# Kernel tuning notes

Measured on AMD Instinct MI355X. Metric: run time of the kernel, lower is better.

The kernel has to match this reference:

```python
import jax, jax.numpy as jnp
import numpy as np

H = 512
V = 50000
S = 400
B = 64


def setup_inputs() -> dict:
    key = jax.random.key(0)
    ks = jax.random.split(key, 20)
    inp = {
        'input': jax.random.normal(ks[0], (1, B, H), jnp.float32),
        'encoder_states': jax.random.normal(ks[1], (S, B, H), jnp.float32),
        'oov_enc_mask': jax.random.randint(ks[2], (S, B), 0, 2, jnp.int32),
        'hidden': jnp.zeros((1, B, H), jnp.float32),
        # GRU params (PyTorch layout: gates ordered r, z, n)
        'W_ih': jax.random.normal(ks[3], (3 * H, H), jnp.float32) * 0.02,
        'W_hh': jax.random.normal(ks[4], (3 * H, H), jnp.float32) * 0.02,
        'b_ih': jax.random.normal(ks[5], (3 * H,), jnp.float32) * 0.02,
        'b_hh': jax.random.normal(ks[6], (3 * H,), jnp.float32) * 0.02,
        # output vocab projection Linear(2H, V)
        'out_W': jax.random.normal(ks[7], (V, 2 * H), jnp.float32) * 0.02,
        'out_b': jax.random.normal(ks[8], (V,), jnp.float32) * 0.02,
        # additive attention params
        'v': jax.random.normal(ks[9], (H, 1), jnp.float32) * 0.02,
        'Wh': jax.random.normal(ks[10], (H, H), jnp.float32) * 0.02,
        'Ws': jax.random.normal(ks[11], (H, H), jnp.float32) * 0.02,
        'b_attn': jax.random.normal(ks[12], (1, H), jnp.float32) * 0.02,
        # pointer probability Linears (H -> 1)
        'pWh': jax.random.normal(ks[13], (1, H), jnp.float32) * 0.02,
        'pWs': jax.random.normal(ks[14], (1, H), jnp.float32) * 0.02,
        'pWx': jax.random.normal(ks[15], (1, H), jnp.float32) * 0.02,
        'pWx_b': jax.random.normal(ks[16], (1,), jnp.float32) * 0.02,
    }
    return inp


def reference(input, encoder_states, oov_enc_mask, hidden,
              W_ih, W_hh, b_ih, b_hh, out_W, out_b,
              v, Wh, Ws, b_attn, pWh, pWs, pWx, pWx_b):
    x = input[0]            # (B, H)
    h0 = hidden[0]          # (B, H)

    # --- single-step GRU (PyTorch gate order r, z, n) ---
    gi = x @ W_ih.T + b_ih      # (B, 3H)
    gh = h0 @ W_hh.T + b_hh     # (B, 3H)
    ir, iz, inn = jnp.split(gi, 3, axis=1)
    hr, hz, hn = jnp.split(gh, 3, axis=1)
    r = jax.nn.sigmoid(ir + hr)
    z = jax.nn.sigmoid(iz + hz)
    n = jnp.tanh(inn + r * hn)
    h = (1.0 - z) * n + z * h0          # decoder_state, (B, H)
    hidden_new = h[None]                # (1, B, H)

    # --- Bahdanau additive attention, softmax over seq axis ---
    x1 = jnp.einsum('sbh,hk->sbk', encoder_states, Wh)   # (S, B, H)
    x2 = h @ Ws                                          # (B, H) broadcasts over S
    scores = jnp.squeeze(jnp.tanh(x1 + x2 + b_attn) @ v, 2)  # (S, B)
    attn = jax.nn.softmax(scores, axis=0)                # (S, B)
    attn_bs = attn.T                                     # (B, S)

    context = jnp.einsum('bs,sbh->bh', attn_bs, encoder_states)  # (B, H)
    global_state = jnp.concatenate([h, context], axis=1)         # (B, 2H)

    # --- pointer probability ---
    p = jax.nn.sigmoid(context @ pWh.T + h @ pWs.T + x @ pWx.T + pWx_b)  # (B, 1)

    vocab_distr = p * jax.nn.selu(global_state @ out_W.T + out_b)        # (B, V)
    oov_vocab_distr = (1.0 - p) * (attn_bs * oov_enc_mask.astype(jnp.float32).T)  # (B, S)
    extended_vocab_distr = jnp.concatenate([vocab_distr, oov_vocab_distr], axis=1)

    return extended_vocab_distr, hidden_new, jnp.squeeze(p), attn
```

## Files before the change

kernel.cpp:

```cpp
#include <hip/hip_runtime.h>
#include <cmath>

#define H    512
#define H2   1024
#define V    50000
#define SEQ  400
#define EXT  (V + SEQ)

typedef __attribute__((ext_vector_type(8))) short short8;
typedef __attribute__((ext_vector_type(4))) float floatx4;

#define LDS_BARRIER() asm volatile("s_waitcnt lgkmcnt(0)\n\ts_barrier" ::: "memory")

__device__ __forceinline__ unsigned int bfpack2(float lo, float hi) {
    unsigned int a = __float_as_uint(lo) + 0x8000u;
    unsigned int b = __float_as_uint(hi) + 0x8000u;
    return __builtin_amdgcn_perm(b, a, 0x07060302);
}
__device__ __forceinline__ uint4 pack8(float4 a, float4 b) {
    uint4 r;
    r.x = bfpack2(a.x, a.y);
    r.y = bfpack2(a.z, a.w);
    r.z = bfpack2(b.x, b.y);
    r.w = bfpack2(b.z, b.w);
    return r;
}
__device__ __forceinline__ float4 ld4(const float* p) { return *(const float4*)p; }

__global__ __launch_bounds__(256) void k0_transpose(
    const float* __restrict__ Wh, const float* __restrict__ Ws,
    unsigned short* __restrict__ WhT, unsigned short* __restrict__ WsT)
{
    __shared__ float T[64][65];
    const float* src = blockIdx.z ? Ws : Wh;
    unsigned short* dst = blockIdx.z ? WsT : WhT;
    const int k0 = blockIdx.x * 64, n0 = blockIdx.y * 64;
    const int tid = threadIdx.x;
    #pragma unroll
    for (int i = 0; i < 16; ++i) {
        int e = i * 256 + tid;
        int r = e >> 6, c = e & 63;
        T[r][c] = src[(size_t)(k0 + r) * H + n0 + c];
    }
    __syncthreads();
    #pragma unroll
    for (int i = 0; i < 16; ++i) {
        int e = i * 256 + tid;
        int nn = e >> 6, kk = e & 63;
        unsigned int u = __float_as_uint(T[kk][nn]) + 0x8000u;
        dst[(size_t)(n0 + nn) * H + k0 + kk] = (unsigned short)(u >> 16);
    }
}

__global__ __launch_bounds__(256) void k1_gru(
    const float* __restrict__ x, const float* __restrict__ h0,
    const float* __restrict__ W_ih, const float* __restrict__ W_hh,
    const float* __restrict__ b_ih, const float* __restrict__ b_hh,
    float* __restrict__ h_out)
{
    __shared__ uint4 Ax[512];
    __shared__ uint4 Ah[512];
    __shared__ uint4 Bg[6][512];
    const int tid  = threadIdx.x;
    const int wave = tid >> 6, lane = tid & 63;
    const int lrow = lane & 15, q = lane >> 4;
    const int J0   = blockIdx.x * 64;

    floatx4 acc[6][4];
    #pragma unroll
    for (int g = 0; g < 6; ++g)
        #pragma unroll
        for (int mt = 0; mt < 4; ++mt) acc[g][mt] = (floatx4){0.f, 0.f, 0.f, 0.f};

    for (int kc = 0; kc < H; kc += 64) {
        __syncthreads();
        #pragma unroll
        for (int c = 0; c < 2; ++c) {
            int idx = c * 256 + tid;
            int m = idx >> 3, j2 = idx & 7, k8 = j2 ^ (m & 7);
            const float* sx = x  + m * H + kc + k8 * 8;
            const float* sh = h0 + m * H + kc + k8 * 8;
            Ax[idx] = pack8(ld4(sx), ld4(sx + 4));
            Ah[idx] = pack8(ld4(sh), ld4(sh + 4));
        }
        #pragma unroll
        for (int g = 0; g < 6; ++g) {
            const float* Wb = (g < 3) ? W_ih : W_hh;
            const int go = (g % 3) * H;
            #pragma unroll
            for (int c = 0; c < 2; ++c) {
                int idx = c * 256 + tid;
                int n = idx >> 3, j2 = idx & 7, k8 = j2 ^ (n & 7);
                const float* sw = Wb + (size_t)(go + J0 + n) * H + kc + k8 * 8;
                Bg[g][idx] = pack8(ld4(sw), ld4(sw + 4));
            }
        }
        __syncthreads();
        #pragma unroll
        for (int kk8 = 0; kk8 < 8; kk8 += 4) {
            const int k8 = kk8 + q;
            short8 ax[4], ah[4];
            #pragma unroll
            for (int mt = 0; mt < 4; ++mt) {
                int m = mt * 16 + lrow;
                ax[mt] = *(const short8*)&Ax[m * 8 + (k8 ^ (m & 7))];
                ah[mt] = *(const short8*)&Ah[m * 8 + (k8 ^ (m & 7))];
            }
            const int n = wave * 16 + lrow;
            const int gidx = n * 8 + (k8 ^ (n & 7));
            #pragma unroll
            for (int g = 0; g < 6; ++g) {
                short8 bb = *(const short8*)&Bg[g][gidx];
                #pragma unroll
                for (int mt = 0; mt < 4; ++mt)
                    acc[g][mt] = __builtin_amdgcn_mfma_f32_16x16x32_bf16(
                        (g < 3) ? ax[mt] : ah[mt], bb, acc[g][mt], 0, 0, 0);
            }
        }
    }
    const int j = J0 + wave * 16 + lrow;
    const float bir = b_ih[j], biz = b_ih[H + j], bin = b_ih[2 * H + j];
    const float bhr = b_hh[j], bhz = b_hh[H + j], bhn = b_hh[2 * H + j];
    #pragma unroll
    for (int mt = 0; mt < 4; ++mt) {
        #pragma unroll
        for (int r = 0; r < 4; ++r) {
            const int bb = mt * 16 + q * 4 + r;
            float rg = 1.f / (1.f + expf(-(acc[0][mt][r] + bir + acc[3][mt][r] + bhr)));
            float zg = 1.f / (1.f + expf(-(acc[1][mt][r] + biz + acc[4][mt][r] + bhz)));
            float ng = tanhf(acc[2][mt][r] + bin + rg * (acc[5][mt][r] + bhn));
            float h0v = h0[bb * H + j];
            h_out[bb * H + j] = (1.f - zg) * ng + zg * h0v;
        }
    }
}

__global__ __launch_bounds__(256) void k2_x2(
    const float* __restrict__ h, const unsigned short* __restrict__ WsT,
    const float* __restrict__ b_attn, float* __restrict__ x2)
{
    __shared__ uint4 Ag[512];
    __shared__ uint4 Bgg[512];
    const int tid  = threadIdx.x;
    const int wave = tid >> 6, lane = tid & 63;
    const int lrow = lane & 15, q = lane >> 4;
    const int n0   = blockIdx.x * 64;

    floatx4 acc[4];
    #pragma unroll
    for (int mt = 0; mt < 4; ++mt) acc[mt] = (floatx4){0.f, 0.f, 0.f, 0.f};

    for (int kc = 0; kc < H; kc += 64) {
        __syncthreads();
        #pragma unroll
        for (int c = 0; c < 2; ++c) {
            int idx = c * 256 + tid;
            int m = idx >> 3, j2 = idx & 7, k8 = j2 ^ (m & 7);
            const float* sh = h + m * H + kc + k8 * 8;
            Ag[idx] = pack8(ld4(sh), ld4(sh + 4));
            int n = m, k8b = j2 ^ (n & 7);
            Bgg[idx] = *(const uint4*)(WsT + (size_t)(n0 + n) * H + kc + k8b * 8);
        }
        __syncthreads();
        #pragma unroll
        for (int kk8 = 0; kk8 < 8; kk8 += 4) {
            const int k8 = kk8 + q;
            const int n = wave * 16 + lrow;
            short8 bb = *(const short8*)&Bgg[n * 8 + (k8 ^ (n & 7))];
            #pragma unroll
            for (int mt = 0; mt < 4; ++mt) {
                int m = mt * 16 + lrow;
                short8 a = *(const short8*)&Ag[m * 8 + (k8 ^ (m & 7))];
                acc[mt] = __builtin_amdgcn_mfma_f32_16x16x32_bf16(a, bb, acc[mt], 0, 0, 0);
            }
        }
    }
    const int n = n0 + wave * 16 + lrow;
    const float ba = b_attn[n];
    #pragma unroll
    for (int mt = 0; mt < 4; ++mt)
        #pragma unroll
        for (int r = 0; r < 4; ++r) {
            const int bb = mt * 16 + q * 4 + r;
            x2[bb * H + n] = acc[mt][r] + ba;
        }
}

__global__ __launch_bounds__(256) void k3_scores(
    const float* __restrict__ enc, const unsigned short* __restrict__ WhT,
    const float* __restrict__ x2, const float* __restrict__ v,
    float* __restrict__ part)
{
    __shared__ uint4 AsG[2][512];
    __shared__ uint4 BsG[2][1024];
    __shared__ float red[256];
    const int s   = blockIdx.x;
    const int nc  = blockIdx.y;
    const int n0  = nc * 128;
    const int tid  = threadIdx.x;
    const int wave = tid >> 6, lane = tid & 63;
    const int lrow = lane & 15, q = lane >> 4;

    const float* Abase = enc + (size_t)s * 64 * H;

    float4 arA[2][2];
    uint4  arB[4];
    #pragma unroll
    for (int c = 0; c < 2; ++c) {
        int idx = c * 256 + tid;
        int m = idx >> 3, k8 = (idx & 7) ^ (m & 7);
        const float* sa = Abase + m * H + k8 * 8;
        arA[c][0] = ld4(sa); arA[c][1] = ld4(sa + 4);
    }
    #pragma unroll
    for (int c = 0; c < 4; ++c) {
        int idx = c * 256 + tid;
        int n = idx >> 3, k8 = (idx & 7) ^ (n & 7);
        arB[c] = *(const uint4*)(WhT + (size_t)(n0 + n) * H + k8 * 8);
    }

    floatx4 acc[4][2];
    #pragma unroll
    for (int mt = 0; mt < 4; ++mt)
        #pragma unroll
        for (int nt = 0; nt < 2; ++nt) acc[mt][nt] = (floatx4){0.f, 0.f, 0.f, 0.f};

    for (int kc = 0; kc < 8; ++kc) {
        const int buf = kc & 1;
        #pragma unroll
        for (int c = 0; c < 2; ++c)
            AsG[buf][c * 256 + tid] = pack8(arA[c][0], arA[c][1]);
        #pragma unroll
        for (int c = 0; c < 4; ++c)
            BsG[buf][c * 256 + tid] = arB[c];
        if (kc < 7) {
            const int ko = (kc + 1) * 64;
            #pragma unroll
            for (int c = 0; c < 2; ++c) {
                int idx = c * 256 + tid;
                int m = idx >> 3, k8 = (idx & 7) ^ (m & 7);
                const float* sa = Abase + m * H + ko + k8 * 8;
                arA[c][0] = ld4(sa); arA[c][1] = ld4(sa + 4);
            }
            #pragma unroll
            for (int c = 0; c < 4; ++c) {
                int idx = c * 256 + tid;
                int n = idx >> 3, k8 = (idx & 7) ^ (n & 7);
                arB[c] = *(const uint4*)(WhT + (size_t)(n0 + n) * H + ko + k8 * 8);
            }
        }
        LDS_BARRIER();
        #pragma unroll
        for (int kk8 = 0; kk8 < 8; kk8 += 4) {
            const int k8 = kk8 + q;
            short8 a[4], b[2];
            #pragma unroll
            for (int mt = 0; mt < 4; ++mt) {
                int m = mt * 16 + lrow;
                a[mt] = *(const short8*)&AsG[buf][m * 8 + (k8 ^ (m & 7))];
            }
            #pragma unroll
            for (int nt = 0; nt < 2; ++nt) {
                int n = wave * 32 + nt * 16 + lrow;
                b[nt] = *(const short8*)&BsG[buf][n * 8 + (k8 ^ (n & 7))];
            }
            #pragma unroll
            for (int mt = 0; mt < 4; ++mt)
                #pragma unroll
                for (int nt = 0; nt < 2; ++nt)
                    acc[mt][nt] = __builtin_amdgcn_mfma_f32_16x16x32_bf16(
                        a[mt], b[nt], acc[mt][nt], 0, 0, 0);
        }
    }
    float val[4][4];
    #pragma unroll
    for (int mt = 0; mt < 4; ++mt) {
        #pragma unroll
        for (int r = 0; r < 4; ++r) {
            const int bb = mt * 16 + q * 4 + r;
            float sum = 0.f;
            #pragma unroll
            for (int nt = 0; nt < 2; ++nt) {
                const int n = n0 + wave * 32 + nt * 16 + lrow;
                sum += tanhf(acc[mt][nt][r] + x2[bb * H + n]) * v[n];
            }
            #pragma unroll
            for (int off = 8; off > 0; off >>= 1) sum += __shfl_down(sum, off, 16);
            val[mt][r] = sum;
        }
    }
    __syncthreads();
    if (lrow == 0) {
        #pragma unroll
        for (int mt = 0; mt < 4; ++mt)
            #pragma unroll
            for (int r = 0; r < 4; ++r)
                red[wave * 64 + mt * 16 + q * 4 + r] = val[mt][r];
    }
    __syncthreads();
    if (tid < 64) {
        float sc = red[tid] + red[64 + tid] + red[128 + tid] + red[192 + tid];
        part[((size_t)nc * SEQ + s) * 64 + tid] = sc;
    }
}

__global__ __launch_bounds__(512) void k4_softmax(
    const float* __restrict__ part, float* __restrict__ attn_out)
{
    const int b = blockIdx.x;
    const int t = threadIdx.x;
    __shared__ float red[8];
    __shared__ float smax, ssum;
    float myv = 0.f, val = -1e30f;
    if (t < SEQ) {
        myv = part[((size_t)0 * SEQ + t) * 64 + b]
            + part[((size_t)1 * SEQ + t) * 64 + b]
            + part[((size_t)2 * SEQ + t) * 64 + b]
            + part[((size_t)3 * SEQ + t) * 64 + b];
        val = myv;
    }
    float m = val;
    #pragma unroll
    for (int off = 32; off > 0; off >>= 1) m = fmaxf(m, __shfl_down(m, off, 64));
    if ((t & 63) == 0) red[t >> 6] = m;
    __syncthreads();
    if (t == 0) {
        float mm = red[0];
        #pragma unroll
        for (int w = 1; w < 8; ++w) mm = fmaxf(mm, red[w]);
        smax = mm;
    }
    __syncthreads();
    float e = (t < SEQ) ? expf(myv - smax) : 0.f;
    float ssv = e;
    #pragma unroll
    for (int off = 32; off > 0; off >>= 1) ssv += __shfl_down(ssv, off, 64);
    if ((t & 63) == 0) red[t >> 6] = ssv;
    __syncthreads();
    if (t == 0) {
        float ss = 0.f;
        #pragma unroll
        for (int w = 0; w < 8; ++w) ss += red[w];
        ssum = ss;
    }
    __syncthreads();
    if (t < SEQ) attn_out[t * 64 + b] = e / ssum;
}

__global__ __launch_bounds__(128) void k5_context(
    const float* __restrict__ enc, const float* __restrict__ attn,
    float* __restrict__ ctxp)
{
    const int b  = blockIdx.x;
    const int hc = blockIdx.y;
    const int sg = blockIdx.z;
    const int t  = threadIdx.x;
    __shared__ float a_s[100];
    if (t < 100) a_s[t] = attn[(sg * 100 + t) * 64 + b];
    __syncthreads();
    const int hh = hc * 128 + t;
    const float* p = enc + ((size_t)(sg * 100) * 64 + b) * H + hh;
    float a0 = 0.f, a1 = 0.f;
    #pragma unroll 5
    for (int i = 0; i < 100; i += 2) {
        a0 += a_s[i]     * p[0];
        a1 += a_s[i + 1] * p[(size_t)64 * H];
        p += (size_t)128 * H;
    }
    ctxp[((size_t)sg * 64 + b) * H + hh] = a0 + a1;
}

__global__ __launch_bounds__(512) void k5b_p(
    const float* __restrict__ ctxp, const float* __restrict__ pWh,
    const float* __restrict__ hdec, const float* __restrict__ pWs,
    const float* __restrict__ x, const float* __restrict__ pWx,
    const float* __restrict__ pWx_b,
    float* __restrict__ ctx, float* __restrict__ p_out, float* __restrict__ p_ws)
{
    const int b = blockIdx.x;
    const int t = threadIdx.x;
    __shared__ float rbuf[8];
    float c = ctxp[((size_t)0 * 64 + b) * H + t]
            + ctxp[((size_t)1 * 64 + b) * H + t]
            + ctxp[((size_t)2 * 64 + b) * H + t]
            + ctxp[((size_t)3 * 64 + b) * H + t];
    ctx[b * H + t] = c;
    float term = c * pWh[t] + hdec[b * H + t] * pWs[t] + x[b * H + t] * pWx[t];
    #pragma unroll
    for (int off = 32; off > 0; off >>= 1) term += __shfl_down(term, off, 64);
    if ((t & 63) == 0) rbuf[t >> 6] = term;
    __syncthreads();
    if (t == 0) {
        float ssv = pWx_b[0];
        #pragma unroll
        for (int w = 0; w < 8; ++w) ssv += rbuf[w];
        float pv = 1.f / (1.f + expf(-ssv));
        p_out[b] = pv;
        p_ws[b]  = pv;
    }
}

__global__ __launch_bounds__(256) void k6_vocab(
    const float* __restrict__ h, const float* __restrict__ ctx,
    const float* __restrict__ outW, const float* __restrict__ outb,
    const float* __restrict__ p_ws, float* __restrict__ ext)
{
    __shared__ uint4 AsG[2][512];
    __shared__ uint4 BsG[2][512];
    __shared__ float p_l[64];
    const int tid  = threadIdx.x;
    const int wave = tid >> 6, lane = tid & 63;
    const int lrow = lane & 15, q = lane >> 4;
    const int v0   = blockIdx.x * 64;

    if (tid < 64) p_l[tid] = p_ws[tid];

    float4 arA[2][2], arB[2][2];
    {
        const float* Ab = h;
        #pragma unroll
        for (int c = 0; c < 2; ++c) {
            int idx = c * 256 + tid;
            int m = idx >> 3, k8 = (idx & 7) ^ (m & 7);
            const float* sa = Ab + m * H + k8 * 8;
            arA[c][0] = ld4(sa); arA[c][1] = ld4(sa + 4);
            int n = m, k8b = (idx & 7) ^ (n & 7);
            int vr = v0 + n; if (vr >= V) vr = V - 1;
            const float* sb = outW + (size_t)vr * H2 + k8b * 8;
            arB[c][0] = ld4(sb); arB[c][1] = ld4(sb + 4);
        }
    }

    floatx4 acc[4];
    #pragma unroll
    for (int mt = 0; mt < 4; ++mt) acc[mt] = (floatx4){0.f, 0.f, 0.f, 0.f};

    for (int kc = 0; kc < 16; ++kc) {
        const int buf = kc & 1;
        #pragma unroll
        for (int c = 0; c < 2; ++c) {
            AsG[buf][c * 256 + tid] = pack8(arA[c][0], arA[c][1]);
            BsG[buf][c * 256 + tid] = pack8(arB[c][0], arB[c][1]);
        }
        if (kc < 15) {
            const int ko = (kc + 1) * 64;
            const float* Ab = (ko < H) ? (h + ko) : (ctx + (ko - H));
            #pragma unroll
            for (int c = 0; c < 2; ++c) {
                int idx = c * 256 + tid;
                int m = idx >> 3, k8 = (idx & 7) ^ (m & 7);
                const float* sa = Ab + m * H + k8 * 8;
                arA[c][0] = ld4(sa); arA[c][1] = ld4(sa + 4);
                int n = m, k8b = (idx & 7) ^ (n & 7);
                int vr = v0 + n; if (vr >= V) vr = V - 1;
                const float* sb = outW + (size_t)vr * H2 + ko + k8b * 8;
                arB[c][0] = ld4(sb); arB[c][1] = ld4(sb + 4);
            }
        }
        LDS_BARRIER();
        #pragma unroll
        for (int kk8 = 0; kk8 < 8; kk8 += 4) {
            const int k8 = kk8 + q;
            const int n = wave * 16 + lrow;
            short8 b = *(const short8*)&BsG[buf][n * 8 + (k8 ^ (n & 7))];
            #pragma unroll
            for (int mt = 0; mt < 4; ++mt) {
                int m = mt * 16 + lrow;
                short8 a = *(const short8*)&AsG[buf][m * 8 + (k8 ^ (m & 7))];
                acc[mt] = __builtin_amdgcn_mfma_f32_16x16x32_bf16(a, b, acc[mt], 0, 0, 0);
            }
        }
    }
    const int n = v0 + wave * 16 + lrow;
    if (n < V) {
        const float ob = outb[n];
        #pragma unroll
        for (int mt = 0; mt < 4; ++mt) {
            #pragma unroll
            for (int r = 0; r < 4; ++r) {
                const int bb = mt * 16 + q * 4 + r;
                float zz = acc[mt][r] + ob;
                float sv = (zz > 0.f) ? 1.0507009873554805f * zz
                                      : 1.7580993408473766f * (expf(zz) - 1.f);
                ext[(size_t)bb * EXT + n] = p_l[bb] * sv;
            }
        }
    }
}

__global__ __launch_bounds__(256) void k7_oov(
    const float* __restrict__ attn, const int* __restrict__ mask,
    const float* __restrict__ p_ws, float* __restrict__ ext)
{
    int e = blockIdx.x * 256 + threadIdx.x;
    if (e < SEQ * 64) {
        int s = e >> 6, b = e & 63;
        float val = (1.f - p_ws[b]) * attn[e] * (mask[e] ? 1.f : 0.f);
        ext[(size_t)b * EXT + V + s] = val;
    }
}

extern "C" void kernel_launch(void* const* d_in, const int* in_sizes, int n_in,
                              void* d_out, int out_size, void* d_ws, size_t ws_size,
                              hipStream_t stream)
{
    (void)in_sizes; (void)n_in; (void)out_size; (void)ws_size;
    const float* x      = (const float*)d_in[0];
    const float* enc    = (const float*)d_in[1];
    const int*   mask   = (const int*)  d_in[2];
    const float* h0     = (const float*)d_in[3];
    const float* W_ih   = (const float*)d_in[4];
    const float* W_hh   = (const float*)d_in[5];
    const float* b_ih   = (const float*)d_in[6];
    const float* b_hh   = (const float*)d_in[7];
    const float* outW   = (const float*)d_in[8];
    const float* outb   = (const float*)d_in[9];
    const float* v      = (const float*)d_in[10];
    const float* Wh     = (const float*)d_in[11];
    const float* Ws     = (const float*)d_in[12];
    const float* b_attn = (const float*)d_in[13];
    const float* pWh    = (const float*)d_in[14];
    const float* pWs    = (const float*)d_in[15];
    const float* pWx    = (const float*)d_in[16];
    const float* pWx_b  = (const float*)d_in[17];

    float* out        = (float*)d_out;
    float* out_ext    = out;
    float* out_hidden = out + (size_t)64 * EXT;
    float* out_p      = out_hidden + 64 * H;
    float* out_attn   = out_p + 64;

    float* ws       = (float*)d_ws;
    float* ws_x2    = ws;
    float* ws_part  = ws_x2 + 64 * H;
    float* ws_ctxp  = ws_part + 4 * SEQ * 64;
    float* ws_ctx   = ws_ctxp + 4 * 64 * H;
    float* ws_p     = ws_ctx + 64 * H;
    unsigned short* ws_whT = (unsigned short*)(ws_p + 64);
    unsigned short* ws_wsT = ws_whT + (size_t)H * H;

    k0_transpose<<<dim3(8, 8, 2), 256, 0, stream>>>(Wh, Ws, ws_whT, ws_wsT);
    k1_gru<<<8, 256, 0, stream>>>(x, h0, W_ih, W_hh, b_ih, b_hh, out_hidden);
    k2_x2<<<8, 256, 0, stream>>>(out_hidden, ws_wsT, b_attn, ws_x2);
    k3_scores<<<dim3(SEQ, 4), 256, 0, stream>>>(enc, ws_whT, ws_x2, v, ws_part);
    k4_softmax<<<64, 512, 0, stream>>>(ws_part, out_attn);
    k5_context<<<dim3(64, 4, 4), 128, 0, stream>>>(enc, out_attn, ws_ctxp);
    k5b_p<<<64, 512, 0, stream>>>(ws_ctxp, pWh, out_hidden, pWs, x, pWx, pWx_b,
                                  ws_ctx, out_p, ws_p);
    k6_vocab<<<(V + 63) / 64, 256, 0, stream>>>(out_hidden, ws_ctx, outW, outb,
                                                ws_p, out_ext);
    k7_oov<<<(SEQ * 64 + 255) / 256, 256, 0, stream>>>(out_attn, mask, ws_p, out_ext);
}
```

Baseline: 520.0 us.

## Split GRU GEMM over K, drop register prefetch, widen vocab tiles

The GRU gate GEMM is split across 8 K-slices in a 2D grid. Partial sums go to a workspace buffer, and a new finalize kernel reduces them and applies the gate nonlinearities, so the 8-block GRU launch no longer underfills the GPU. The k3 scores and k6 vocab kernels lose their register-prefetch double buffering and return to simple single-buffered LDS loops. k6 now computes 128 vocab columns per block with two N-subtiles per wave, which reuses the activation tile more but overlaps loads with compute less and launches half as many blocks. The split GRU adds an extra kernel launch and roughly 6 MB of workspace traffic.

New measurement: 463.8 us. -10.8%, faster.

```diff
diff --git a/kernel.cpp b/kernel.cpp
--- a/kernel.cpp
+++ b/kernel.cpp
@@ -9,8 +9,6 @@
 
 typedef __attribute__((ext_vector_type(8))) short short8;
 typedef __attribute__((ext_vector_type(4))) float floatx4;
-
-#define LDS_BARRIER() asm volatile("s_waitcnt lgkmcnt(0)\n\ts_barrier" ::: "memory")
 
 __device__ __forceinline__ unsigned int bfpack2(float lo, float hi) {
     unsigned int a = __float_as_uint(lo) + 0x8000u;
@@ -52,11 +50,10 @@
     }
 }
 
-__global__ __launch_bounds__(256) void k1_gru(
+__global__ __launch_bounds__(256) void k1_gru_part(
     const float* __restrict__ x, const float* __restrict__ h0,
     const float* __restrict__ W_ih, const float* __restrict__ W_hh,
-    const float* __restrict__ b_ih, const float* __restrict__ b_hh,
-    float* __restrict__ h_out)
+    float* __restrict__ gacc)
 {
     __shared__ uint4 Ax[512];
     __shared__ uint4 Ah[512];
@@ -65,74 +62,96 @@
     const int wave = tid >> 6, lane = tid & 63;
     const int lrow = lane & 15, q = lane >> 4;
     const int J0   = blockIdx.x * 64;
-
-    floatx4 acc[6][4];
-    #pragma unroll
-    for (int g = 0; g < 6; ++g)
-        #pragma unroll
-        for (int mt = 0; mt < 4; ++mt) acc[g][mt] = (floatx4){0.f, 0.f, 0.f, 0.f};
-
-    for (int kc = 0; kc < H; kc += 64) {
-        __syncthreads();
+    const int ks   = blockIdx.y;
+    const int kc   = ks * 64;
+
+    #pragma unroll
+    for (int c = 0; c < 2; ++c) {
+        int idx = c * 256 + tid;
+        int m = idx >> 3, j2 = idx & 7, k8 = j2 ^ (m & 7);
+        const float* sx = x  + m * H + kc + k8 * 8;
+        const float* sh = h0 + m * H + kc + k8 * 8;
+        Ax[idx] = pack8(ld4(sx), ld4(sx + 4));
+        Ah[idx] = pack8(ld4(sh), ld4(sh + 4));
+    }
+    #pragma unroll
+    for (int g = 0; g < 6; ++g) {
+        const float* Wb = (g < 3) ? W_ih : W_hh;
+        const int go = (g % 3) * H;
         #pragma unroll
         for (int c = 0; c < 2; ++c) {
             int idx = c * 256 + tid;
-            int m = idx >> 3, j2 = idx & 7, k8 = j2 ^ (m & 7);
-            const float* sx = x  + m * H + kc + k8 * 8;
-            const float* sh = h0 + m * H + kc + k8 * 8;
-            Ax[idx] = pack8(ld4(sx), ld4(sx + 4));
-            Ah[idx] = pack8(ld4(sh), ld4(sh + 4));
-        }
+            int n = idx >> 3, j2 = idx & 7, k8 = j2 ^ (n & 7);
+            const float* sw = Wb + (size_t)(go + J0 + n) * H + kc + k8 * 8;
+            Bg[g][idx] = pack8(ld4(sw), ld4(sw + 4));
+        }
+    }
+    __syncthreads();
+
+    floatx4 acc[6];
+    #pragma unroll
+    for (int g = 0; g < 6; ++g) acc[g] = (floatx4){0.f, 0.f, 0.f, 0.f};
+    floatx4 accm[6][4];
+    #pragma unroll
+    for (int g = 0; g < 6; ++g)
+        #pragma unroll
+        for (int mt = 0; mt < 4; ++mt) accm[g][mt] = (floatx4){0.f, 0.f, 0.f, 0.f};
+
+    #pragma unroll
+    for (int kk8 = 0; kk8 < 8; kk8 += 4) {
+        const int k8 = kk8 + q;
+        short8 ax[4], ah[4];
+        #pragma unroll
+        for (int mt = 0; mt < 4; ++mt) {
+            int m = mt * 16 + lrow;
+            ax[mt] = *(const short8*)&Ax[m * 8 + (k8 ^ (m & 7))];
+            ah[mt] = *(const short8*)&Ah[m * 8 + (k8 ^ (m & 7))];
+        }
+        const int n = wave * 16 + lrow;
+        const int gidx = n * 8 + (k8 ^ (n & 7));
         #pragma unroll
         for (int g = 0; g < 6; ++g) {
-            const float* Wb = (g < 3) ? W_ih : W_hh;
-            const int go = (g % 3) * H;
-            #pragma unroll
-            for (int c = 0; c < 2; ++c) {
-                int idx = c * 256 + tid;
-                int n = idx >> 3, j2 = idx & 7, k8 = j2 ^ (n & 7);
-                const float* sw = Wb + (size_t)(go + J0 + n) * H + kc + k8 * 8;
-                Bg[g][idx] = pack8(ld4(sw), ld4(sw + 4));
-            }
-        }
-        __syncthreads();
-        #pragma unroll
-        for (int kk8 = 0; kk8 < 8; kk8 += 4) {
-            const int k8 = kk8 + q;
-            short8 ax[4], ah[4];
-            #pragma unroll
-            for (int mt = 0; mt < 4; ++mt) {
-                int m = mt * 16 + lrow;
-                ax[mt] = *(const short8*)&Ax[m * 8 + (k8 ^ (m & 7))];
-                ah[mt] = *(const short8*)&Ah[m * 8 + (k8 ^ (m & 7))];
-            }
-            const int n = wave * 16 + lrow;
-            const int gidx = n * 8 + (k8 ^ (n & 7));
-            #pragma unroll
-            for (int g = 0; g < 6; ++g) {
-                short8 bb = *(const short8*)&Bg[g][gidx];
-                #pragma unroll
-                for (int mt = 0; mt < 4; ++mt)
-                    acc[g][mt] = __builtin_amdgcn_mfma_f32_16x16x32_bf16(
-                        (g < 3) ? ax[mt] : ah[mt], bb, acc[g][mt], 0, 0, 0);
-            }
+            short8 bb = *(const short8*)&Bg[g][gidx];
+            #pragma unroll
+            for (int mt = 0; mt < 4; ++mt)
+                accm[g][mt] = __builtin_amdgcn_mfma_f32_16x16x32_bf16(
+                    (g < 3) ? ax[mt] : ah[mt], bb, accm[g][mt], 0, 0, 0);
         }
     }
     const int j = J0 + wave * 16 + lrow;
-    const float bir = b_ih[j], biz = b_ih[H + j], bin = b_ih[2 * H + j];
-    const float bhr = b_hh[j], bhz = b_hh[H + j], bhn = b_hh[2 * H + j];
-    #pragma unroll
-    for (int mt = 0; mt < 4; ++mt) {
-        #pragma unroll
-        for (int r = 0; r < 4; ++r) {
-            const int bb = mt * 16 + q * 4 + r;
-            float rg = 1.f / (1.f + expf(-(acc[0][mt][r] + bir + acc[3][mt][r] + bhr)));
-            float zg = 1.f / (1.f + expf(-(acc[1][mt][r] + biz + acc[4][mt][r] + bhz)));
-            float ng = tanhf(acc[2][mt][r] + bin + rg * (acc[5][mt][r] + bhn));
-            float h0v = h0[bb * H + j];
-            h_out[bb * H + j] = (1.f - zg) * ng + zg * h0v;
-        }
-    }
+    #pragma unroll
+    for (int g = 0; g < 6; ++g)
+        #pragma unroll
+        for (int mt = 0; mt < 4; ++mt)
+            #pragma unroll
+            for (int r = 0; r < 4; ++r) {
+                const int bb = mt * 16 + q * 4 + r;
+                gacc[(((size_t)g * 8 + ks) * 64 + bb) * H + j] = accm[g][mt][r];
+            }
+}
+
+__global__ __launch_bounds__(256) void k1_gru_fin(
+    const float* __restrict__ gacc, const float* __restrict__ h0,
+    const float* __restrict__ b_ih, const float* __restrict__ b_hh,
+    float* __restrict__ h_out)
+{
+    const int e = blockIdx.x * 256 + threadIdx.x;
+    const int j = e & (H - 1);
+    const int b = e >> 9;
+    float gs[6];
+    #pragma unroll
+    for (int g = 0; g < 6; ++g) {
+        float sum = 0.f;
+        #pragma unroll
+        for (int ks = 0; ks < 8; ++ks)
+            sum += gacc[(((size_t)g * 8 + ks) * 64 + b) * H + j];
+        gs[g] = sum;
+    }
+    float rg = 1.f / (1.f + expf(-(gs[0] + b_ih[j] + gs[3] + b_hh[j])));
+    float zg = 1.f / (1.f + expf(-(gs[1] + b_ih[H + j] + gs[4] + b_hh[H + j])));
+    float ng = tanhf(gs[2] + b_ih[2 * H + j] + rg * (gs[5] + b_hh[2 * H + j]));
+    float h0v = h0[b * H + j];
+    h_out[b * H + j] = (1.f - zg) * ng + zg * h0v;
 }
 
 __global__ __launch_bounds__(256) void k2_x2(
@@ -158,8 +177,7 @@
             int m = idx >> 3, j2 = idx & 7, k8 = j2 ^ (m & 7);
             const float* sh = h + m * H + kc + k8 * 8;
             Ag[idx] = pack8(ld4(sh), ld4(sh + 4));
-            int n = m, k8b = j2 ^ (n & 7);
-            Bgg[idx] = *(const uint4*)(WsT + (size_t)(n0 + n) * H + kc + k8b * 8);
+            Bgg[idx] = *(const uint4*)(WsT + (size_t)(n0 + m) * H + kc + k8 * 8);
         }
         __syncthreads();
         #pragma unroll
@@ -191,8 +209,8 @@
     const float* __restrict__ x2, const float* __restrict__ v,
     float* __restrict__ part)
 {
-    __shared__ uint4 AsG[2][512];
-    __shared__ uint4 BsG[2][1024];
+    __shared__ uint4 AsG[512];
+    __shared__ uint4 BsG[1024];
     __shared__ float red[256];
     const int s   = blockIdx.x;
     const int nc  = blockIdx.y;
@@ -201,55 +219,29 @@
     const int wave = tid >> 6, lane = tid & 63;
     const int lrow = lane & 15, q = lane >> 4;
 
+    floatx4 acc[4][2];
+    #pragma unroll
+    for (int mt = 0; mt < 4; ++mt)
+        #pragma unroll
+        for (int nt = 0; nt < 2; ++nt) acc[mt][nt] = (floatx4){0.f, 0.f, 0.f, 0.f};
+
     const float* Abase = enc + (size_t)s * 64 * H;
-
-    float4 arA[2][2];
-    uint4  arB[4];
-    #pragma unroll
-    for (int c = 0; c < 2; ++c) {
-        int idx = c * 256 + tid;
-        int m = idx >> 3, k8 = (idx & 7) ^ (m & 7);
-        const float* sa = Abase + m * H + k8 * 8;
-        arA[c][0] = ld4(sa); arA[c][1] = ld4(sa + 4);
-    }
-    #pragma unroll
-    for (int c = 0; c < 4; ++c) {
-        int idx = c * 256 + tid;
-        int n = idx >> 3, k8 = (idx & 7) ^ (n & 7);
-        arB[c] = *(const uint4*)(WhT + (size_t)(n0 + n) * H + k8 * 8);
-    }
-
-    floatx4 acc[4][2];
-    #pragma unroll
-    for (int mt = 0; mt < 4; ++mt)
-        #pragma unroll
-        for (int nt = 0; nt < 2; ++nt) acc[mt][nt] = (floatx4){0.f, 0.f, 0.f, 0.f};
-
-    for (int kc = 0; kc < 8; ++kc) {
-        const int buf = kc & 1;
-        #pragma unroll
-        for (int c = 0; c < 2; ++c)
-            AsG[buf][c * 256 + tid] = pack8(arA[c][0], arA[c][1]);
-        #pragma unroll
-        for (int c = 0; c < 4; ++c)
-            BsG[buf][c * 256 + tid] = arB[c];
-        if (kc < 7) {
-            const int ko = (kc + 1) * 64;
-            #pragma unroll
-            for (int c = 0; c < 2; ++c) {
-                int idx = c * 256 + tid;
-                int m = idx >> 3, k8 = (idx & 7) ^ (m & 7);
-                const float* sa = Abase + m * H + ko + k8 * 8;
-                arA[c][0] = ld4(sa); arA[c][1] = ld4(sa + 4);
-            }
-            #pragma unroll
-            for (int c = 0; c < 4; ++c) {
-                int idx = c * 256 + tid;
-                int n = idx >> 3, k8 = (idx & 7) ^ (n & 7);
-                arB[c] = *(const uint4*)(WhT + (size_t)(n0 + n) * H + ko + k8 * 8);
-            }
-        }
-        LDS_BARRIER();
+    for (int kc = 0; kc < H; kc += 64) {
+        __syncthreads();
+        #pragma unroll
+        for (int c = 0; c < 2; ++c) {
+            int idx = c * 256 + tid;
+            int m = idx >> 3, k8 = (idx & 7) ^ (m & 7);
+            const float* sa = Abase + m * H + kc + k8 * 8;
+            AsG[idx] = pack8(ld4(sa), ld4(sa + 4));
+        }
+        #pragma unroll
+        for (int c = 0; c < 4; ++c) {
+            int idx = c * 256 + tid;
+            int n = idx >> 3, k8 = (idx & 7) ^ (n & 7);
+            BsG[idx] = *(const uint4*)(WhT + (size_t)(n0 + n) * H + kc + k8 * 8);
+        }
+        __syncthreads();
         #pragma unroll
         for (int kk8 = 0; kk8 < 8; kk8 += 4) {
             const int k8 = kk8 + q;
@@ -257,12 +249,12 @@
             #pragma unroll
             for (int mt = 0; mt < 4; ++mt) {
                 int m = mt * 16 + lrow;
-                a[mt] = *(const short8*)&AsG[buf][m * 8 + (k8 ^ (m & 7))];
+                a[mt] = *(const short8*)&AsG[m * 8 + (k8 ^ (m & 7))];
             }
             #pragma unroll
             for (int nt = 0; nt < 2; ++nt) {
                 int n = wave * 32 + nt * 16 + lrow;
-                b[nt] = *(const short8*)&BsG[buf][n * 8 + (k8 ^ (n & 7))];
+                b[nt] = *(const short8*)&BsG[n * 8 + (k8 ^ (n & 7))];
             }
             #pragma unroll
             for (int mt = 0; mt < 4; ++mt)
@@ -405,84 +397,78 @@
     const float* __restrict__ outW, const float* __restrict__ outb,
     const float* __restrict__ p_ws, float* __restrict__ ext)
 {
-    __shared__ uint4 AsG[2][512];
-    __shared__ uint4 BsG[2][512];
+    __shared__ uint4 AsG[512];
+    __shared__ uint4 BsG[1024];
     __shared__ float p_l[64];
     const int tid  = threadIdx.x;
     const int wave = tid >> 6, lane = tid & 63;
     const int lrow = lane & 15, q = lane >> 4;
-    const int v0   = blockIdx.x * 64;
+    const int v0   = blockIdx.x * 128;
 
     if (tid < 64) p_l[tid] = p_ws[tid];
 
-    float4 arA[2][2], arB[2][2];
-    {
-        const float* Ab = h;
+    floatx4 acc[4][2];
+    #pragma unroll
+    for (int mt = 0; mt < 4; ++mt)
+        #pragma unroll
+        for (int nt = 0; nt < 2; ++nt) acc[mt][nt] = (floatx4){0.f, 0.f, 0.f, 0.f};
+
+    for (int kc = 0; kc < H2; kc += 64) {
+        __syncthreads();
+        const float* Ab = (kc < H) ? (h + kc) : (ctx + (kc - H));
         #pragma unroll
         for (int c = 0; c < 2; ++c) {
             int idx = c * 256 + tid;
             int m = idx >> 3, k8 = (idx & 7) ^ (m & 7);
             const float* sa = Ab + m * H + k8 * 8;
-            arA[c][0] = ld4(sa); arA[c][1] = ld4(sa + 4);
-            int n = m, k8b = (idx & 7) ^ (n & 7);
+            AsG[idx] = pack8(ld4(sa), ld4(sa + 4));
+        }
+        #pragma unroll
+        for (int c = 0; c < 4; ++c) {
+            int idx = c * 256 + tid;
+            int n = idx >> 3, k8 = (idx & 7) ^ (n & 7);
             int vr = v0 + n; if (vr >= V) vr = V - 1;
-            const float* sb = outW + (size_t)vr * H2 + k8b * 8;
-            arB[c][0] = ld4(sb); arB[c][1] = ld4(sb + 4);
-        }
-    }
-
-    floatx4 acc[4];
-    #pragma unroll
-    for (int mt = 0; mt < 4; ++mt) acc[mt] = (floatx4){0.f, 0.f, 0.f, 0.f};
-
-    for (int kc = 0; kc < 16; ++kc) {
-        const int buf = kc & 1;
-        #pragma unroll
-        for (int c = 0; c < 2; ++c) {
-            AsG[buf][c * 256 + tid] = pack8(arA[c][0], arA[c][1]);
-            BsG[buf][c * 256 + tid] = pack8(arB[c][0], arB[c][1]);
-        }
-        if (kc < 15) {
-            const int ko = (kc + 1) * 64;
-            const float* Ab = (ko < H) ? (h + ko) : (ctx + (ko - H));
-            #pragma unroll
-            for (int c = 0; c < 2; ++c) {
-                int idx = c * 256 + tid;
-                int m = idx >> 3, k8 = (idx & 7) ^ (m & 7);
-                const float* sa = Ab + m * H + k8 * 8;
-                arA[c][0] = ld4(sa); arA[c][1] = ld4(sa + 4);
-                int n = m, k8b = (idx & 7) ^ (n & 7);
-                int vr = v0 + n; if (vr >= V) vr = V - 1;
-                const float* sb = outW + (size_t)vr * H2 + ko + k8b * 8;
-                arB[c][0] = ld4(sb); arB[c][1] = ld4(sb + 4);
-            }
-        }
-        LDS_BARRIER();
+            const float* sb = outW + (size_t)vr * H2 + kc + k8 * 8;
+            BsG[idx] = pack8(ld4(sb), ld4(sb + 4));
+        }
+        __syncthreads();
         #pragma unroll
         for (int kk8 = 0; kk8 < 8; kk8 += 4) {
             const int k8 = kk8 + q;
-            const int n = wave * 16 + lrow;
-            short8 b = *(const short8*)&BsG[buf][n * 8 + (k8 ^ (n & 7))];
+            short8 a[4], b[2];
             #pragma unroll
             for (int mt = 0; mt < 4; ++mt) {
                 int m = mt * 16 + lrow;
-                short8 a = *(const short8*)&AsG[buf][m * 8 + (k8 ^ (m & 7))];
-                acc[mt] = __builtin_amdgcn_mfma_f32_16x16x32_bf16(a, b, acc[mt], 0, 0, 0);
-            }
-        }
-    }
-    const int n = v0 + wave * 16 + lrow;
-    if (n < V) {
-        const float ob = outb[n];
-        #pragma unroll
-        for (int mt = 0; mt < 4; ++mt) {
-            #pragma unroll
-            for (int r = 0; r < 4; ++r) {
-                const int bb = mt * 16 + q * 4 + r;
-                float zz = acc[mt][r] + ob;
-                float sv = (zz > 0.f) ? 1.0507009873554805f * zz
-                                      : 1.7580993408473766f * (expf(zz) - 1.f);
-                ext[(size_t)bb * EXT + n] = p_l[bb] * sv;
+                a[mt] = *(const short8*)&AsG[m * 8 + (k8 ^ (m & 7))];
+            }
+            #pragma unroll
+            for (int nt = 0; nt < 2; ++nt) {
+                int n = wave * 32 + nt * 16 + lrow;
+                b[nt] = *(const short8*)&BsG[n * 8 + (k8 ^ (n & 7))];
+            }
+            #pragma unroll
+            for (int mt = 0; mt < 4; ++mt)
+                #pragma unroll
+                for (int nt = 0; nt < 2; ++nt)
+                    acc[mt][nt] = __builtin_amdgcn_mfma_f32_16x16x32_bf16(
+                        a[mt], b[nt], acc[mt][nt], 0, 0, 0);
+        }
+    }
+    #pragma unroll
+    for (int nt = 0; nt < 2; ++nt) {
+        const int n = v0 + wave * 32 + nt * 16 + lrow;
+        if (n < V) {
+            const float ob = outb[n];
+            #pragma unroll
+            for (int mt = 0; mt < 4; ++mt) {
+                #pragma unroll
+                for (int r = 0; r < 4; ++r) {
+                    const int bb = mt * 16 + q * 4 + r;
+                    float zz = acc[mt][nt][r] + ob;
+                    float sv = (zz > 0.f) ? 1.0507009873554805f * zz
+                                          : 1.7580993408473766f * (expf(zz) - 1.f);
+                    ext[(size_t)bb * EXT + n] = p_l[bb] * sv;
+                }
             }
         }
     }
@@ -536,18 +522,20 @@
     float* ws_ctxp  = ws_part + 4 * SEQ * 64;
     float* ws_ctx   = ws_ctxp + 4 * 64 * H;
     float* ws_p     = ws_ctx + 64 * H;
-    unsigned short* ws_whT = (unsigned short*)(ws_p + 64);
+    float* ws_gacc  = ws_p + 64;
+    unsigned short* ws_whT = (unsigned short*)(ws_gacc + 6 * 8 * 64 * H);
     unsigned short* ws_wsT = ws_whT + (size_t)H * H;
 
     k0_transpose<<<dim3(8, 8, 2), 256, 0, stream>>>(Wh, Ws, ws_whT, ws_wsT);
-    k1_gru<<<8, 256, 0, stream>>>(x, h0, W_ih, W_hh, b_ih, b_hh, out_hidden);
+    k1_gru_part<<<dim3(8, 8), 256, 0, stream>>>(x, h0, W_ih, W_hh, ws_gacc);
+    k1_gru_fin<<<128, 256, 0, stream>>>(ws_gacc, h0, b_ih, b_hh, out_hidden);
     k2_x2<<<8, 256, 0, stream>>>(out_hidden, ws_wsT, b_attn, ws_x2);
     k3_scores<<<dim3(SEQ, 4), 256, 0, stream>>>(enc, ws_whT, ws_x2, v, ws_part);
     k4_softmax<<<64, 512, 0, stream>>>(ws_part, out_attn);
     k5_context<<<dim3(64, 4, 4), 128, 0, stream>>>(enc, out_attn, ws_ctxp);
     k5b_p<<<64, 512, 0, stream>>>(ws_ctxp, pWh, out_hidden, pWs, x, pWx, pWx_b,
                                   ws_ctx, out_p, ws_p);
-    k6_vocab<<<(V + 63) / 64, 256, 0, stream>>>(out_hidden, ws_ctx, outW, outb,
-                                                ws_p, out_ext);
+    k6_vocab<<<(V + 127) / 128, 256, 0, stream>>>(out_hidden, ws_ctx, outW, outb,
+                                                  ws_p, out_ext);
     k7_oov<<<(SEQ * 64 + 255) / 256, 256, 0, stream>>>(out_attn, mask, ws_p, out_ext);
 }
```
